# Performance work log

Measured on AMD Instinct MI355X. Metric: run time of the kernel, lower is better.

Reference implementation:

```python
import jax, jax.numpy as jnp
import numpy as np

B, N, FIN, H, D = 4, 2048, 128, 4, 64
ALPHA = 0.2  # LeakyReLU negative slope


def _xavier_uniform(key, shape):
    fan_in, fan_out = shape[0], shape[1]
    limit = float(np.sqrt(6.0 / (fan_in + fan_out)))
    return jax.random.uniform(key, shape, jnp.float32, -limit, limit)


def setup_inputs() -> dict:
    key = jax.random.key(0)
    k1, k2, k3, k4 = jax.random.split(key, 4)
    x = jax.random.normal(k1, (B, N, FIN), jnp.float32)
    adj = jax.random.randint(k2, (B, N, N), 0, 2, jnp.int32)  # dense 0/1 mask
    W = _xavier_uniform(k3, (FIN, H * D))
    a = _xavier_uniform(k4, (2 * D, 1))
    return {"x": x, "adj": adj, "W": W, "a": a}


def reference(x, adj, W, a):
    Bb, Nn, _ = x.shape
    Dd = a.shape[0] // 2
    Hh = W.shape[1] // Dd
    # h: [B, N, H, D]
    h = (x @ W).reshape(Bb, Nn, Hh, Dd)
    # Additive attention: e[b,i,j,h] = leakyrelu(a1 . h[b,i,h] + a2 . h[b,j,h])
    a1 = a[:Dd, 0]
    a2 = a[Dd:, 0]
    ei = jnp.einsum('bnhd,d->bnh', h, a1)  # source (row i) term
    ej = jnp.einsum('bnhd,d->bnh', h, a2)  # dest (col j) term
    e = ei[:, :, None, :] + ej[:, None, :, :]  # [B, N, N, H]
    e = jnp.where(e >= 0, e, ALPHA * e)  # LeakyReLU
    e = jnp.where(adj[..., None] == 0, -jnp.inf, e)
    att = jax.nn.softmax(e, axis=2)  # softmax over neighbors j
    # dropout is a no-op in eval mode (training=False)
    out = jnp.einsum('bijh,bjhd->bihd', att, h)  # [B, N, H, D]
    return out.mean(axis=2)  # mean over heads -> [B, N, D]
```

## Files before the change

kernel.cpp:

```cpp
#include <hip/hip_runtime.h>

#define NN 2048
#define NH 4
#define DD 64
#define FIN 128
#define NB 4
#define LOG2E 1.44269504f

typedef unsigned short u16;
typedef unsigned int u32;
typedef short sh8 __attribute__((ext_vector_type(8)));
typedef float f32x4 __attribute__((ext_vector_type(4)));

static __device__ __forceinline__ u16 f2bf(float f) {
    u32 u = __builtin_bit_cast(u32, f);
    u += 0x7fffu + ((u >> 16) & 1u);
    return (u16)(u >> 16);
}
static __device__ __forceinline__ u32 pk_bf(float a, float b) {
    u32 ua = __builtin_bit_cast(u32, a) + 0x8000u;
    u32 ub = __builtin_bit_cast(u32, b) + 0x8000u;
    return __builtin_amdgcn_perm(ub, ua, 0x07060302u);
}
static __device__ __forceinline__ float fast_exp2(float x) {
    float r;
    asm("v_exp_f32 %0, %1" : "=v"(r) : "v"(x));
    return r;
}

static __device__ __forceinline__ void cd_probe(int ln15, int q, int* irow, int* icol) {
    sh8 pa, pb, qa, qb;
    #pragma unroll
    for (int ii = 0; ii < 8; ++ii) {
        pa[ii] = (short)f2bf((float)ln15);
        pb[ii] = 0;
        qa[ii] = 0;
        qb[ii] = (short)f2bf((float)ln15);
    }
    if (q == 0) { pb[0] = (short)f2bf(1.0f); qa[0] = (short)f2bf(1.0f); }
    f32x4 z = {};
    f32x4 prow = __builtin_amdgcn_mfma_f32_16x16x32_bf16(pa, pb, z, 0, 0, 0);
    f32x4 pcol = __builtin_amdgcn_mfma_f32_16x16x32_bf16(qa, qb, z, 0, 0, 0);
    #pragma unroll
    for (int r = 0; r < 4; ++r) {
        irow[r] = (int)(prow[r] + 0.5f);
        icol[r] = (int)(pcol[r] + 0.5f);
    }
}


__global__ __launch_bounds__(256)
void k_prep(const float* __restrict__ W, u16* __restrict__ WT) {
    const int bt  = blockIdx.x;
    const int kt  = bt & 3;
    const int ct8 = bt >> 2;
    __shared__ float tile[32][33];
    const int tid = threadIdx.x;
    const int rr = tid >> 5, cc = tid & 31;
    #pragma unroll
    for (int i = 0; i < 4; ++i)
        tile[rr + 8 * i][cc] = W[(size_t)(kt * 32 + rr + 8 * i) * 256 + ct8 * 32 + cc];
    __syncthreads();
    #pragma unroll
    for (int i = 0; i < 4; ++i)
        WT[(size_t)(ct8 * 32 + rr + 8 * i) * FIN + kt * 32 + cc] = f2bf(tile[cc][rr + 8 * i]);
}

__global__ __launch_bounds__(256)
void k_gemm_h(const float* __restrict__ x, const u16* __restrict__ WT,
              const float* __restrict__ a,
              u16* __restrict__ hTf, float* __restrict__ ei_g, float* __restrict__ ej_g) {
    const int nb = blockIdx.x, b = blockIdx.y;
    const int tid = threadIdx.x, hd = tid >> 6, lane = tid & 63, ln15 = lane & 15, q = lane >> 4;
    const int q8 = q * 8;
    const int n0 = nb * 64;

    __shared__ u16 xs[64][136];
    __shared__ float cs[NH][4][16][20];
    {
        const int col = (tid & 31) * 4;
        const int r0  = tid >> 5;
        #pragma unroll
        for (int rr = 0; rr < 8; ++rr) {
            const int row = r0 + rr * 8;
            const float4 v = *(const float4*)(x + ((size_t)(b * NN + n0 + row)) * FIN + col);
            *(u32*)&xs[row][col]     = pk_bf(v.x, v.y);
            *(u32*)&xs[row][col + 2] = pk_bf(v.z, v.w);
        }
    }
    __syncthreads();

    int irow[4], icol[4];
    cd_probe(ln15, q, irow, icol);

    f32x4 acc[4][4] = {};
    #pragma unroll
    for (int ks = 0; ks < 4; ++ks) {
        sh8 af[4], bfr[4];
        #pragma unroll
        for (int ct = 0; ct < 4; ++ct)
            af[ct] = *(const sh8*)(WT + (size_t)(hd * 64 + ct * 16 + ln15) * FIN + ks * 32 + q8);
        #pragma unroll
        for (int nt = 0; nt < 4; ++nt)
            bfr[nt] = *(const sh8*)&xs[nt * 16 + ln15][ks * 32 + q8];
        #pragma unroll
        for (int ct = 0; ct < 4; ++ct)
            #pragma unroll
            for (int nt = 0; nt < 4; ++nt)
                acc[ct][nt] = __builtin_amdgcn_mfma_f32_16x16x32_bf16(af[ct], bfr[nt], acc[ct][nt], 0, 0, 0);
    }

    float eip[4] = {}, ejq[4] = {};
    #pragma unroll
    for (int ct = 0; ct < 4; ++ct) {
        #pragma unroll
        for (int nt = 0; nt < 4; ++nt)
            #pragma unroll
            for (int r = 0; r < 4; ++r)
                cs[hd][nt][irow[r]][icol[r]] = acc[ct][nt][r];

        #pragma unroll
        for (int p = 0; p < 2; ++p) {
            const float4 c0 = *(const float4*)&cs[hd][2 * p + (q >> 1)][ln15][(q & 1) * 8];
            const float4 c1 = *(const float4*)&cs[hd][2 * p + (q >> 1)][ln15][(q & 1) * 8 + 4];
            uint4 o;
            o.x = pk_bf(c0.x, c0.y); o.y = pk_bf(c0.z, c0.w);
            o.z = pk_bf(c1.x, c1.y); o.w = pk_bf(c1.z, c1.w);
            *(uint4*)(hTf + ((((size_t)(b * NH + hd) * 64 + nb * 2 + p) * 4 + ct) * 512) + lane * 8) = o;
        }

        float a1v[4], a2v[4];
        #pragma unroll
        for (int r = 0; r < 4; ++r) {
            const int d = ct * 16 + 4 * q + r;
            a1v[r] = a[d] * LOG2E;
            a2v[r] = a[64 + d] * LOG2E;
        }
        #pragma unroll
        for (int nt = 0; nt < 4; ++nt)
            #pragma unroll
            for (int r = 0; r < 4; ++r) {
                const float v = cs[hd][nt][4 * q + r][ln15];
                eip[nt] += v * a1v[r];
                ejq[nt] += v * a2v[r];
            }
    }
    #pragma unroll
    for (int nt = 0; nt < 4; ++nt) {
        eip[nt] += __shfl_xor(eip[nt], 16);
        eip[nt] += __shfl_xor(eip[nt], 32);
        ejq[nt] += __shfl_xor(ejq[nt], 16);
        ejq[nt] += __shfl_xor(ejq[nt], 32);
    }
    if (lane < 16) {
        const size_t bhd = (size_t)(b * NH + hd) * NN;
        #pragma unroll
        for (int nt = 0; nt < 4; ++nt) {
            ei_g[bhd + n0 + nt * 16 + lane] = eip[nt];
            ej_g[bhd + n0 + nt * 16 + lane] = ejq[nt];
        }
    }
}

template <int NJT>
__global__ __launch_bounds__(256, 3)
void k_attn(const int* __restrict__ adj, const u16* __restrict__ hTf,
            const float* __restrict__ ei_g, const float* __restrict__ ej_g,
            float* __restrict__ o_part, float* __restrict__ l_part) {
    const int ib = blockIdx.x, js = blockIdx.y, b = blockIdx.z;
    const int js_n = gridDim.y;
    const int tid = threadIdx.x, hd = tid >> 6, lane = tid & 63, ln15 = lane & 15, q = lane >> 4;
    const int q8 = q * 8;
    const int iA = ib * 32 + ln15;
    const int jt0 = js * NJT;

    __shared__ u32 mlds[32][65];

    {
        const int row = (hd << 3) + (lane >> 3);
        const int* abase = adj + (size_t)(b * NN + ib * 32 + row) * NN + jt0 * 32 + (lane & 7) * 4;
        #pragma unroll
        for (int jb = 0; jb < NJT; jb += 8) {
            int4 vv[8];
            #pragma unroll
            for (int u = 0; u < 8; ++u)
                vv[u] = *(const int4*)(abase + (jb + u) * 32);
            #pragma unroll
            for (int u = 0; u < 8; ++u) {
                u32 nib = (vv[u].x ? 1u : 0u) | (vv[u].y ? 2u : 0u) |
                          (vv[u].z ? 4u : 0u) | (vv[u].w ? 8u : 0u);
                u32 w = nib << (4 * (lane & 7));
                w |= __shfl_xor(w, 1);
                w |= __shfl_xor(w, 2);
                w |= __shfl_xor(w, 4);
                if ((lane & 7) == 0) mlds[row][jb + u] = w;
            }
        }
    }
    __syncthreads();

    int irow[4], icol[4];
    cd_probe(ln15, q, irow, icol);

    const size_t bhd = (size_t)(b * NH + hd) * NN;
    const float eivA = ei_g[bhd + iA];
    const float eivB = ei_g[bhd + iA + 16];
    const float* ejp  = ej_g + bhd + q8;
    const u16*   hfp  = hTf + (size_t)(b * NH + hd) * (64 * 2048) + (size_t)lane * 8;

    sh8 ones;
    #pragma unroll
    for (int ii = 0; ii < 8; ++ii) ones[ii] = (short)0x3F80;

    f32x4 acc[8] = {};
    f32x4 accl[2] = {};

    u32 mA = mlds[ln15][0];
    u32 mB = mlds[ln15 + 16][0];
    float4 e0 = *(const float4*)(ejp + jt0 * 32);
    float4 e1 = *(const float4*)(ejp + jt0 * 32 + 4);
    sh8 h0 = *(const sh8*)(hfp + (size_t)jt0 * 2048);
    sh8 h1 = *(const sh8*)(hfp + (size_t)jt0 * 2048 + 512);
    sh8 h2 = *(const sh8*)(hfp + (size_t)jt0 * 2048 + 1024);
    sh8 h3 = *(const sh8*)(hfp + (size_t)jt0 * 2048 + 1536);

    for (int t = 0; t < NJT; ++t) {
        const int tn = (t + 1 < NJT) ? jt0 + t + 1 : jt0;
        const int tl = (t + 1 < NJT) ? t + 1 : 0;
        const u32 mAn = mlds[ln15][tl];
        const u32 mBn = mlds[ln15 + 16][tl];
        const float4 e0n = *(const float4*)(ejp + tn * 32);
        const float4 e1n = *(const float4*)(ejp + tn * 32 + 4);
        const sh8 h0n = *(const sh8*)(hfp + (size_t)tn * 2048);
        const sh8 h1n = *(const sh8*)(hfp + (size_t)tn * 2048 + 512);
        const sh8 h2n = *(const sh8*)(hfp + (size_t)tn * 2048 + 1024);
        const sh8 h3n = *(const sh8*)(hfp + (size_t)tn * 2048 + 1536);

        const float ef[8] = { e0.x, e0.y, e0.z, e0.w, e1.x, e1.y, e1.z, e1.w };
        const u32 mqA = mA >> q8;
        const u32 mqB = mB >> q8;
        float pA[8], pB[8];
        #pragma unroll
        for (int ii = 0; ii < 8; ++ii) {
            float eA = eivA + ef[ii];
            float eB = eivB + ef[ii];
            eA = fmaxf(eA, 0.2f * eA);
            eB = fmaxf(eB, 0.2f * eB);
            const float xA = fast_exp2(eA);
            const float xB = fast_exp2(eB);
            pA[ii] = (mqA & (1u << ii)) ? xA : 0.f;
            pB[ii] = (mqB & (1u << ii)) ? xB : 0.f;
        }
        union { uint4 u; sh8 v; } avA, avB;
        avA.u.x = pk_bf(pA[0], pA[1]); avA.u.y = pk_bf(pA[2], pA[3]);
        avA.u.z = pk_bf(pA[4], pA[5]); avA.u.w = pk_bf(pA[6], pA[7]);
        avB.u.x = pk_bf(pB[0], pB[1]); avB.u.y = pk_bf(pB[2], pB[3]);
        avB.u.z = pk_bf(pB[4], pB[5]); avB.u.w = pk_bf(pB[6], pB[7]);

        acc[0] = __builtin_amdgcn_mfma_f32_16x16x32_bf16(avA.v, h0, acc[0], 0, 0, 0);
        acc[1] = __builtin_amdgcn_mfma_f32_16x16x32_bf16(avA.v, h1, acc[1], 0, 0, 0);
        acc[2] = __builtin_amdgcn_mfma_f32_16x16x32_bf16(avA.v, h2, acc[2], 0, 0, 0);
        acc[3] = __builtin_amdgcn_mfma_f32_16x16x32_bf16(avA.v, h3, acc[3], 0, 0, 0);
        accl[0] = __builtin_amdgcn_mfma_f32_16x16x32_bf16(avA.v, ones, accl[0], 0, 0, 0);
        acc[4] = __builtin_amdgcn_mfma_f32_16x16x32_bf16(avB.v, h0, acc[4], 0, 0, 0);
        acc[5] = __builtin_amdgcn_mfma_f32_16x16x32_bf16(avB.v, h1, acc[5], 0, 0, 0);
        acc[6] = __builtin_amdgcn_mfma_f32_16x16x32_bf16(avB.v, h2, acc[6], 0, 0, 0);
        acc[7] = __builtin_amdgcn_mfma_f32_16x16x32_bf16(avB.v, h3, acc[7], 0, 0, 0);
        accl[1] = __builtin_amdgcn_mfma_f32_16x16x32_bf16(avB.v, ones, accl[1], 0, 0, 0);

        mA = mAn; mB = mBn; e0 = e0n; e1 = e1n;
        h0 = h0n; h1 = h1n; h2 = h2n; h3 = h3n;
    }

    const size_t pbA = (((size_t)b * 128 + ib * 2 + 0) * js_n + js) * NH + hd;
    const size_t pbB = (((size_t)b * 128 + ib * 2 + 1) * js_n + js) * NH + hd;
    #pragma unroll
    for (int r = 0; r < 4; ++r) {
        l_part[pbA * 16 + irow[r]] = accl[0][r];
        l_part[pbB * 16 + irow[r]] = accl[1][r];
    }
    float* opA = o_part + pbA * 1024;
    float* opB = o_part + pbB * 1024;
    #pragma unroll
    for (int dt = 0; dt < 4; ++dt)
        #pragma unroll
        for (int r = 0; r < 4; ++r) {
            opA[(size_t)irow[r] * 64 + dt * 16 + icol[r]] = acc[dt][r];
            opB[(size_t)irow[r] * 64 + dt * 16 + icol[r]] = acc[4 + dt][r];
        }
}

template <int JS>
__global__ __launch_bounds__(256)
void k_combine(const float* __restrict__ o_part, const float* __restrict__ l_part,
               float* __restrict__ out) {
    const int ib = blockIdx.x, b = blockIdx.y;
    const int tid = threadIdx.x;
    const int i = tid >> 4, d4 = (tid & 15) * 4;
    float  lv[NH][JS];
    float4 ov[NH][JS];
    #pragma unroll
    for (int h = 0; h < NH; ++h)
        #pragma unroll
        for (int js = 0; js < JS; ++js) {
            const size_t pbase = (((size_t)b * 128 + ib) * JS + js) * NH + h;
            lv[h][js] = l_part[pbase * 16 + i];
            ov[h][js] = *(const float4*)(o_part + pbase * 1024 + (size_t)i * 64 + d4);
        }
    float4 sacc = {0.f, 0.f, 0.f, 0.f};
    #pragma unroll
    for (int h = 0; h < NH; ++h) {
        float l = 0.f;
        float4 oh = {0.f, 0.f, 0.f, 0.f};
        #pragma unroll
        for (int js = 0; js < JS; ++js) {
            l += lv[h][js];
            oh.x += ov[h][js].x; oh.y += ov[h][js].y;
            oh.z += ov[h][js].z; oh.w += ov[h][js].w;
        }
        const float inv = 0.25f / l;
        sacc.x += oh.x * inv; sacc.y += oh.y * inv;
        sacc.z += oh.z * inv; sacc.w += oh.w * inv;
    }
    *(float4*)(out + ((size_t)(b * NN) + ib * 16 + i) * DD + d4) = sacc;
}

extern "C" void kernel_launch(void* const* d_in, const int* in_sizes, int n_in,
                              void* d_out, int out_size, void* d_ws, size_t ws_size,
                              hipStream_t stream) {
    const float* x = nullptr; const int* adj = nullptr;
    const float* W = nullptr; const float* a = nullptr;
    for (int i = 0; i < n_in; ++i) {
        switch (in_sizes[i]) {
            case NB * NN * FIN:  x   = (const float*)d_in[i]; break;
            case NB * NN * NN:   adj = (const int*)d_in[i];   break;
            case FIN * 256:      W   = (const float*)d_in[i]; break;
            case 2 * DD:         a   = (const float*)d_in[i]; break;
            default: break;
        }
    }
    if (!x)   x   = (const float*)d_in[0];
    if (!adj) adj = (const int*)d_in[1];
    if (!W)   W   = (const float*)d_in[2];
    if (!a)   a   = (const float*)d_in[3];
    float* out = (float*)d_out;

    char* ws = (char*)d_ws;
    u16*   WT  = (u16*)(ws);
    float* ei  = (float*)(ws + 65536);
    float* ej  = (float*)(ws + 196608);
    u16*   hTf = (u16*)(ws + 327680);
    float* l_p = (float*)(ws + 6619136);
    float* o_p = (float*)(ws + 7143424);

    const size_t need4 = 7143424 + (size_t)4 * 8388608;
    const size_t need2 = 7143424 + (size_t)2 * 8388608;
    const int js_n = (ws_size >= need4) ? 4 : (ws_size >= need2) ? 2 : 1;

    k_prep<<<dim3(32), dim3(256), 0, stream>>>(W, WT);
    k_gemm_h<<<dim3(32, NB), dim3(256), 0, stream>>>(x, WT, a, hTf, ei, ej);
    if (js_n == 4)
        k_attn<16><<<dim3(64, 4, NB), dim3(256), 0, stream>>>(adj, hTf, ei, ej, o_p, l_p);
    else if (js_n == 2)
        k_attn<32><<<dim3(64, 2, NB), dim3(256), 0, stream>>>(adj, hTf, ei, ej, o_p, l_p);
    else
        k_attn<64><<<dim3(64, 1, NB), dim3(256), 0, stream>>>(adj, hTf, ei, ej, o_p, l_p);
    if (js_n == 4)      k_combine<4><<<dim3(128, NB), dim3(256), 0, stream>>>(o_p, l_p, out);
    else if (js_n == 2) k_combine<2><<<dim3(128, NB), dim3(256), 0, stream>>>(o_p, l_p, out);
    else                k_combine<1><<<dim3(128, NB), dim3(256), 0, stream>>>(o_p, l_p, out);
}
```

Measured before the change: 138.2 us.

## Stage ej in LDS, double-buffer h loads two tiles ahead, raise occupancy

```diff
diff --git a/kernel.cpp b/kernel.cpp
--- a/kernel.cpp
+++ b/kernel.cpp
@@ -163,7 +163,7 @@
 }
 
 template <int NJT>
-__global__ __launch_bounds__(256, 3)
+__global__ __launch_bounds__(256, 4)
 void k_attn(const int* __restrict__ adj, const u16* __restrict__ hTf,
             const float* __restrict__ ei_g, const float* __restrict__ ej_g,
             float* __restrict__ o_part, float* __restrict__ l_part) {
@@ -174,7 +174,8 @@
     const int iA = ib * 32 + ln15;
     const int jt0 = js * NJT;
 
-    __shared__ u32 mlds[32][65];
+    __shared__ u32 mlds[32][NJT + 1];
+    __shared__ float ejs[NH][NJT * 32];
 
     {
         const int row = (hd << 3) + (lane >> 3);
@@ -197,16 +198,23 @@
             }
         }
     }
+    const size_t bhd = (size_t)(b * NH + hd) * NN;
+    {
+        const float* src = ej_g + bhd + jt0 * 32;
+        #pragma unroll
+        for (int u = 0; u < NJT / 8; ++u) {
+            const int o4 = (u * 64 + lane) * 4;
+            *(float4*)&ejs[hd][o4] = *(const float4*)(src + o4);
+        }
+    }
     __syncthreads();
 
     int irow[4], icol[4];
     cd_probe(ln15, q, irow, icol);
 
-    const size_t bhd = (size_t)(b * NH + hd) * NN;
     const float eivA = ei_g[bhd + iA];
     const float eivB = ei_g[bhd + iA + 16];
-    const float* ejp  = ej_g + bhd + q8;
-    const u16*   hfp  = hTf + (size_t)(b * NH + hd) * (64 * 2048) + (size_t)lane * 8;
+    const u16*  hfp  = hTf + (size_t)(b * NH + hd) * (64 * 2048) + (size_t)lane * 8;
 
     sh8 ones;
     #pragma unroll
@@ -215,26 +223,19 @@
     f32x4 acc[8] = {};
     f32x4 accl[2] = {};
 
-    u32 mA = mlds[ln15][0];
-    u32 mB = mlds[ln15 + 16][0];
-    float4 e0 = *(const float4*)(ejp + jt0 * 32);
-    float4 e1 = *(const float4*)(ejp + jt0 * 32 + 4);
-    sh8 h0 = *(const sh8*)(hfp + (size_t)jt0 * 2048);
-    sh8 h1 = *(const sh8*)(hfp + (size_t)jt0 * 2048 + 512);
-    sh8 h2 = *(const sh8*)(hfp + (size_t)jt0 * 2048 + 1024);
-    sh8 h3 = *(const sh8*)(hfp + (size_t)jt0 * 2048 + 1536);
-
+    sh8 H[2][4];
+    #pragma unroll
+    for (int s = 0; s < 2; ++s)
+        #pragma unroll
+        for (int k = 0; k < 4; ++k)
+            H[s][k] = *(const sh8*)(hfp + (size_t)(jt0 + s) * 2048 + k * 512);
+
+    #pragma unroll
     for (int t = 0; t < NJT; ++t) {
-        const int tn = (t + 1 < NJT) ? jt0 + t + 1 : jt0;
-        const int tl = (t + 1 < NJT) ? t + 1 : 0;
-        const u32 mAn = mlds[ln15][tl];
-        const u32 mBn = mlds[ln15 + 16][tl];
-        const float4 e0n = *(const float4*)(ejp + tn * 32);
-        const float4 e1n = *(const float4*)(ejp + tn * 32 + 4);
-        const sh8 h0n = *(const sh8*)(hfp + (size_t)tn * 2048);
-        const sh8 h1n = *(const sh8*)(hfp + (size_t)tn * 2048 + 512);
-        const sh8 h2n = *(const sh8*)(hfp + (size_t)tn * 2048 + 1024);
-        const sh8 h3n = *(const sh8*)(hfp + (size_t)tn * 2048 + 1536);
+        const u32 mA = mlds[ln15][t];
+        const u32 mB = mlds[ln15 + 16][t];
+        const float4 e0 = *(const float4*)&ejs[hd][t * 32 + q8];
+        const float4 e1 = *(const float4*)&ejs[hd][t * 32 + q8 + 4];
 
         const float ef[8] = { e0.x, e0.y, e0.z, e0.w, e1.x, e1.y, e1.z, e1.w };
         const u32 mqA = mA >> q8;
@@ -257,19 +258,22 @@
         avB.u.x = pk_bf(pB[0], pB[1]); avB.u.y = pk_bf(pB[2], pB[3]);
         avB.u.z = pk_bf(pB[4], pB[5]); avB.u.w = pk_bf(pB[6], pB[7]);
 
-        acc[0] = __builtin_amdgcn_mfma_f32_16x16x32_bf16(avA.v, h0, acc[0], 0, 0, 0);
-        acc[1] = __builtin_amdgcn_mfma_f32_16x16x32_bf16(avA.v, h1, acc[1], 0, 0, 0);
-        acc[2] = __builtin_amdgcn_mfma_f32_16x16x32_bf16(avA.v, h2, acc[2], 0, 0, 0);
-        acc[3] = __builtin_amdgcn_mfma_f32_16x16x32_bf16(avA.v, h3, acc[3], 0, 0, 0);
+        acc[0] = __builtin_amdgcn_mfma_f32_16x16x32_bf16(avA.v, H[t & 1][0], acc[0], 0, 0, 0);
+        acc[1] = __builtin_amdgcn_mfma_f32_16x16x32_bf16(avA.v, H[t & 1][1], acc[1], 0, 0, 0);
+        acc[2] = __builtin_amdgcn_mfma_f32_16x16x32_bf16(avA.v, H[t & 1][2], acc[2], 0, 0, 0);
+        acc[3] = __builtin_amdgcn_mfma_f32_16x16x32_bf16(avA.v, H[t & 1][3], acc[3], 0, 0, 0);
         accl[0] = __builtin_amdgcn_mfma_f32_16x16x32_bf16(avA.v, ones, accl[0], 0, 0, 0);
-        acc[4] = __builtin_amdgcn_mfma_f32_16x16x32_bf16(avB.v, h0, acc[4], 0, 0, 0);
-        acc[5] = __builtin_amdgcn_mfma_f32_16x16x32_bf16(avB.v, h1, acc[5], 0, 0, 0);
-        acc[6] = __builtin_amdgcn_mfma_f32_16x16x32_bf16(avB.v, h2, acc[6], 0, 0, 0);
-        acc[7] = __builtin_amdgcn_mfma_f32_16x16x32_bf16(avB.v, h3, acc[7], 0, 0, 0);
+        acc[4] = __builtin_amdgcn_mfma_f32_16x16x32_bf16(avB.v, H[t & 1][0], acc[4], 0, 0, 0);
+        acc[5] = __builtin_amdgcn_mfma_f32_16x16x32_bf16(avB.v, H[t & 1][1], acc[5], 0, 0, 0);
+        acc[6] = __builtin_amdgcn_mfma_f32_16x16x32_bf16(avB.v, H[t & 1][2], acc[6], 0, 0, 0);
+        acc[7] = __builtin_amdgcn_mfma_f32_16x16x32_bf16(avB.v, H[t & 1][3], acc[7], 0, 0, 0);
         accl[1] = __builtin_amdgcn_mfma_f32_16x16x32_bf16(avB.v, ones, accl[1], 0, 0, 0);
 
-        mA = mAn; mB = mBn; e0 = e0n; e1 = e1n;
-        h0 = h0n; h1 = h1n; h2 = h2n; h3 = h3n;
+        if (t + 2 < NJT) {
+            #pragma unroll
+            for (int k = 0; k < 4; ++k)
+                H[t & 1][k] = *(const sh8*)(hfp + (size_t)(jt0 + t + 2) * 2048 + k * 512);
+        }
     }
 
     const size_t pbA = (((size_t)b * 128 + ib * 2 + 0) * js_n + js) * NH + hd;
@@ -297,16 +301,6 @@
     const int ib = blockIdx.x, b = blockIdx.y;
     const int tid = threadIdx.x;
     const int i = tid >> 4, d4 = (tid & 15) * 4;
-    float  lv[NH][JS];
-    float4 ov[NH][JS];
-    #pragma unroll
-    for (int h = 0; h < NH; ++h)
-        #pragma unroll
-        for (int js = 0; js < JS; ++js) {
-            const size_t pbase = (((size_t)b * 128 + ib) * JS + js) * NH + h;
-            lv[h][js] = l_part[pbase * 16 + i];
-            ov[h][js] = *(const float4*)(o_part + pbase * 1024 + (size_t)i * 64 + d4);
-        }
     float4 sacc = {0.f, 0.f, 0.f, 0.f};
     #pragma unroll
     for (int h = 0; h < NH; ++h) {
@@ -314,9 +308,10 @@
         float4 oh = {0.f, 0.f, 0.f, 0.f};
         #pragma unroll
         for (int js = 0; js < JS; ++js) {
-            l += lv[h][js];
-            oh.x += ov[h][js].x; oh.y += ov[h][js].y;
-            oh.z += ov[h][js].z; oh.w += ov[h][js].w;
+            const size_t pbase = (((size_t)b * 128 + ib) * JS + js) * NH + h;
+            l += l_part[pbase * 16 + i];
+            const float4 ov = *(const float4*)(o_part + pbase * 1024 + (size_t)i * 64 + d4);
+            oh.x += ov.x; oh.y += ov.y; oh.z += ov.z; oh.w += ov.w;
         }
         const float inv = 0.25f / l;
         sacc.x += oh.x * inv; sacc.y += oh.y * inv;
```

Measured after the change: 136.9 us. About the same (-0.9%).
